# Kernel tuning notes

Hardware: AMD Instinct MI355X
Metric: run time of the kernel (lower is better)

## Reference

```python
import jax, jax.numpy as jnp
import numpy as np

NUM_HEADS = 16
NUM_KV_HEADS = 4
ROPE_THETA = 10000.0


def apply_rope(x, position_ids, theta):
    # x: [B, S, h, d]; position_ids: [B, S]
    d = x.shape[-1]
    freqs = 1.0 / theta ** (jnp.arange(0, d, 2, dtype=jnp.float32) / d)  # [d/2]
    angles = position_ids.astype(jnp.float32)[..., None] * freqs          # [B, S, d/2]
    cos = jnp.cos(angles)[:, :, None, :]                                  # [B, S, 1, d/2]
    sin = jnp.sin(angles)[:, :, None, :]
    xr = x.astype(jnp.float32).reshape(*x.shape[:-1], d // 2, 2)
    x0, x1 = xr[..., 0], xr[..., 1]
    o0 = x0 * cos - x1 * sin
    o1 = x0 * sin + x1 * cos
    out = jnp.stack((o0, o1), axis=-1).reshape(*x.shape)
    return out.astype(x.dtype)


def setup_inputs() -> dict:
    key = jax.random.key(0)
    k0, k1, k2, k3, k4 = jax.random.split(key, 5)
    B, S, H = 1, 2048, 2048
    Hkv = H // (NUM_HEADS // NUM_KV_HEADS)  # 512
    init_scale = 0.02 / np.sqrt(H)
    return {
        "hidden_states": jax.random.normal(k0, (B, S, H), jnp.float32),
        "attention_mask": jnp.ones((B, S), jnp.int32),
        "segment_ids": jnp.zeros((B, S), jnp.int32),
        "position_ids": jnp.broadcast_to(jnp.arange(S, dtype=jnp.int32)[None], (B, S)),
        "Wq": jax.random.normal(k1, (H, H), jnp.float32) * init_scale,
        "Wk": jax.random.normal(k2, (H, Hkv), jnp.float32) * init_scale,
        "Wv": jax.random.normal(k3, (H, Hkv), jnp.float32) * init_scale,
        "Wo": jax.random.normal(k4, (H, H), jnp.float32) * init_scale,
    }


def reference(hidden_states, attention_mask, segment_ids, position_ids, Wq, Wk, Wv, Wo):
    B, S, H = hidden_states.shape
    nh, nkv = NUM_HEADS, NUM_KV_HEADS
    g = nh // nkv
    hd = H // nh

    xq = (hidden_states @ Wq).reshape(B, S, nh, hd)
    xk = (hidden_states @ Wk).reshape(B, S, nkv, hd)
    xv = (hidden_states @ Wv).reshape(B, S, nkv, hd)
    # GQA repeat: 'b s (h d) -> b s (h g) d' == repeat each kv head g times contiguously
    xk = jnp.repeat(xk, g, axis=2)  # [B, S, nh, hd]
    xv = jnp.repeat(xv, g, axis=2)

    xq = apply_rope(xq, position_ids, ROPE_THETA)
    xk = apply_rope(xk, position_ids, ROPE_THETA)

    # masks: causal AND padding AND segment
    causal = jnp.tril(jnp.ones((S, S), dtype=bool))[None, None]            # [1,1,S,S]
    pad = (attention_mask > 0)[:, None, None, :]                            # [B,1,1,S]
    seg = (segment_ids[:, :, None] == segment_ids[:, None, :])[:, None]     # [B,1,S,S]
    mask = causal & pad & seg                                               # [B,1,S,S]

    scale = 1.0 / np.sqrt(hd)
    logits = jnp.einsum("bqhd,bkhd->bhqk", xq.astype(jnp.float32), xk.astype(jnp.float32)) * scale
    logits = jnp.where(mask, logits, jnp.finfo(jnp.float32).min)
    probs = jax.nn.softmax(logits, axis=-1).astype(xv.dtype)
    attn = jnp.einsum("bhqk,bkhd->bqhd", probs, xv)                         # [B,S,nh,hd]

    out = attn.reshape(B, S, H) @ Wo
    return out
```

## Files before the change

### kernel.cpp

```cpp
#include <hip/hip_runtime.h>
#include <hip/hip_bf16.h>
#include <stdint.h>
#include <math.h>

#define SS 2048
#define HH 2048
#define NH 16
#define NKV 4
#define HD 128
#define HKV 512
#define NQKV 3072

typedef __bf16 bf16x8 __attribute__((ext_vector_type(8)));
typedef float f32x4 __attribute__((ext_vector_type(4)));

static_assert(sizeof(bf16x8) == 16, "bf16x8 must be 16B");

__device__ __forceinline__ void async_ld16(const void* gp, void* lp) {
  __builtin_amdgcn_global_load_lds(
      (const __attribute__((address_space(1))) unsigned int*)(uintptr_t)gp,
      (__attribute__((address_space(3))) unsigned int*)(uintptr_t)lp,
      16, 0, 0);
}

__device__ __forceinline__ unsigned short f2bu(float f) {
  __hip_bfloat16 b = __float2bfloat16(f);
  return *reinterpret_cast<unsigned short*>(&b);
}

__global__ __launch_bounds__(256) void k_prep1(
    const float* __restrict__ X, const float* __restrict__ Wq, const float* __restrict__ Wk,
    const float* __restrict__ Wv, const float* __restrict__ Wo,
    const int* __restrict__ amv, const int* __restrict__ seg, int* __restrict__ kseg,
    float2* __restrict__ rtab,
    __hip_bfloat16* __restrict__ Xb, __hip_bfloat16* __restrict__ WqT,
    __hip_bfloat16* __restrict__ WkT, __hip_bfloat16* __restrict__ WvT,
    __hip_bfloat16* __restrict__ WoT) {
  __shared__ float tile[32][33];
  int b = blockIdx.x;
  if (b < 4096) {
    int i = b * 256 + threadIdx.y * 32 + threadIdx.x;
    float4 v = ((const float4*)X)[i];
    ushort4 o;
    o.x = f2bu(v.x); o.y = f2bu(v.y); o.z = f2bu(v.z); o.w = f2bu(v.w);
    ((ushort4*)Xb)[i] = o;
    return;
  }
  b -= 4096;
  if (b >= 10248) {
    int i = (b - 10248) * 256 + threadIdx.y * 32 + threadIdx.x;
    int p = i >> 6, f = i & 63;
    const float L2T_D64 = 0.20762050593046837f;
    float freq = exp2f(-L2T_D64 * (float)f);
    float sn, cs;
    sincosf((float)p * freq, &sn, &cs);
    rtab[i] = make_float2(sn, cs);
    return;
  }
  if (b >= 10240) {
    int i = (b - 10240) * 256 + threadIdx.y * 32 + threadIdx.x;
    kseg[i] = (amv[i] > 0) ? seg[i] : 0x7fffffff;
    return;
  }
  const float* src; __hip_bfloat16* dst; int xtiles;
  if (b < 4096)      { src = Wq; dst = WqT; xtiles = 64; }
  else if (b < 8192) { src = Wo; dst = WoT; xtiles = 64; b -= 4096; }
  else if (b < 9216) { src = Wk; dst = WkT; xtiles = 16; b -= 8192; }
  else               { src = Wv; dst = WvT; xtiles = 16; b -= 9216; }
  const int C = xtiles * 32;
  int bx = (b % xtiles) * 32;
  int by = (b / xtiles) * 32;
  int tx = threadIdx.x, ty = threadIdx.y;
#pragma unroll
  for (int i = 0; i < 4; i++)
    tile[ty + i * 8][tx] = src[(size_t)(by + ty + i * 8) * C + bx + tx];
  __syncthreads();
#pragma unroll
  for (int i = 0; i < 4; i++)
    dst[(size_t)(bx + ty + i * 8) * HH + by + tx] = __float2bfloat16(tile[tx][ty + i * 8]);
}

__global__ __launch_bounds__(256, 2) void k_gemm_qkv(
    const __hip_bfloat16* __restrict__ A, const __hip_bfloat16* __restrict__ B,
    __hip_bfloat16* __restrict__ Qb, __hip_bfloat16* __restrict__ Kb,
    __hip_bfloat16* __restrict__ Vt, const int* __restrict__ pos,
    const float2* __restrict__ rtab) {
  __shared__ __align__(16) __hip_bfloat16 sA0[64 * 64];
  __shared__ __align__(16) __hip_bfloat16 sA1[64 * 64];
  __shared__ __align__(16) __hip_bfloat16 sA2[64 * 64];
  __shared__ __align__(16) __hip_bfloat16 sB0[128 * 64];
  __shared__ __align__(16) __hip_bfloat16 sB1[128 * 64];
  __shared__ __align__(16) __hip_bfloat16 sB2[128 * 64];
  const int tid = threadIdx.x;
  const int lane = tid & 63;
  const int wave = tid >> 6;
  const int bm = blockIdx.y * 64;
  const int bn = blockIdx.x * 128;
  const int wm = (wave & 1) * 32;
  const int wn = (wave >> 1) * 64;
  const int am = lane & 15;
  const int ch = lane >> 4;

  f32x4 acc[2][4] = {};

  auto stage = [&](__hip_bfloat16* sA, __hip_bfloat16* sB, int k0) {
#pragma unroll
    for (int q = 0; q < 2; q++) {
      int c = q * 256 + tid;
      int row = c >> 3, kp = c & 7;
      int col = (kp ^ (row & 7)) * 8;
      async_ld16(A + (size_t)(bm + row) * HH + k0 + col, (char*)sA + c * 16);
    }
#pragma unroll
    for (int q = 0; q < 4; q++) {
      int c = q * 256 + tid;
      int row = c >> 3, kp = c & 7;
      int col = (kp ^ (row & 7)) * 8;
      async_ld16(B + (size_t)(bn + row) * HH + k0 + col, (char*)sB + c * 16);
    }
  };
  auto compute = [&](const __hip_bfloat16* sA, const __hip_bfloat16* sB) {
#pragma unroll
    for (int kb = 0; kb < 2; kb++) {
      bf16x8 a[2], b[4];
#pragma unroll
      for (int i = 0; i < 2; i++) {
        int row = wm + i * 16 + am;
        a[i] = *(const bf16x8*)(sA + row * 64 + (((kb * 4 + ch) ^ (row & 7)) * 8));
      }
#pragma unroll
      for (int j = 0; j < 4; j++) {
        int row = wn + j * 16 + am;
        b[j] = *(const bf16x8*)(sB + row * 64 + (((kb * 4 + ch) ^ (row & 7)) * 8));
      }
#pragma unroll
      for (int i = 0; i < 2; i++)
#pragma unroll
        for (int j = 0; j < 4; j++)
          acc[i][j] = __builtin_amdgcn_mfma_f32_16x16x32_bf16(a[i], b[j], acc[i][j], 0, 0, 0);
    }
  };

  __hip_bfloat16 *cA = sA0, *nA = sA1, *fA = sA2;
  __hip_bfloat16 *cB = sB0, *nB = sB1, *fB = sB2;
  stage(cA, cB, 0);
  stage(nA, nB, 64);
  for (int t = 0; t < 32; ++t) {
    if (t + 1 < 32) asm volatile("s_waitcnt vmcnt(6)" ::: "memory");
    else            asm volatile("s_waitcnt vmcnt(0)" ::: "memory");
    asm volatile("s_barrier" ::: "memory");
    if (t + 2 < 32) stage(fA, fB, (t + 2) * 64);
    compute(cA, cB);
    __hip_bfloat16* tp;
    tp = cA; cA = nA; nA = fA; fA = tp;
    tp = cB; cB = nB; nB = fB; fB = tp;
  }

  const bool isV = (bn >= HH + HKV);
  if (isV) {
#pragma unroll
    for (int j = 0; j < 4; j++) {
      int lc = bn + wn + j * 16 + am - (HH + HKV);
#pragma unroll
      for (int i = 0; i < 2; i++) {
        int row = bm + wm + i * 16 + ch * 4;
        ushort4 o;
        o.x = f2bu(acc[i][j][0]); o.y = f2bu(acc[i][j][1]);
        o.z = f2bu(acc[i][j][2]); o.w = f2bu(acc[i][j][3]);
        *(ushort4*)(Vt + (size_t)lc * SS + row) = o;
      }
    }
  } else {
    const float SCLQ = 0.08838834764831845f * 1.4426950408889634f;
    const bool isQ = (bn < HH);
    int pint[2][4];
#pragma unroll
    for (int i = 0; i < 2; i++)
#pragma unroll
      for (int r = 0; r < 4; r++)
        pint[i][r] = pos[bm + wm + i * 16 + ch * 4 + r];
    const float sgn = (am & 1) ? 1.0f : -1.0f;
#pragma unroll
    for (int j = 0; j < 4; j++) {
      int col = bn + wn + j * 16 + am;
      int lc = isQ ? col : (col - HH);
      int fidx = (lc >> 1) & 63;
#pragma unroll
      for (int i = 0; i < 2; i++)
#pragma unroll
        for (int r = 0; r < 4; r++) {
          float v = acc[i][j][r];
          float px = __shfl_xor(v, 1, 64);
          float2 sc = rtab[pint[i][r] * 64 + fidx];
          float o = v * sc.y + sgn * px * sc.x;
          int row = bm + wm + i * 16 + ch * 4 + r;
          if (isQ) Qb[(size_t)row * HH + col] = __float2bfloat16(o * SCLQ);
          else     Kb[(size_t)row * HKV + lc] = __float2bfloat16(o);
        }
    }
  }
}

__global__ __launch_bounds__(256, 3) void k_gemm_out(
    const __hip_bfloat16* __restrict__ A, const __hip_bfloat16* __restrict__ B,
    float* __restrict__ C) {
  __shared__ __align__(16) __hip_bfloat16 sA0[64 * 64];
  __shared__ __align__(16) __hip_bfloat16 sB0[128 * 64];
  __shared__ __align__(16) __hip_bfloat16 sA1[64 * 64];
  __shared__ __align__(16) __hip_bfloat16 sB1[128 * 64];
  const int tid = threadIdx.x;
  const int lane = tid & 63;
  const int wave = tid >> 6;
  const int bm = blockIdx.y * 64;
  const int bn = blockIdx.x * 128;
  const int wm = (wave & 1) * 32;
  const int wn = (wave >> 1) * 64;
  const int am = lane & 15;
  const int ch = lane >> 4;

  f32x4 acc[2][4] = {};

  auto stage = [&](__hip_bfloat16* sA, __hip_bfloat16* sB, int k0) {
#pragma unroll
    for (int q = 0; q < 2; q++) {
      int c = q * 256 + tid;
      int row = c >> 3, kp = c & 7;
      int col = (kp ^ (row & 7)) * 8;
      async_ld16(A + (size_t)(bm + row) * HH + k0 + col, (char*)sA + c * 16);
    }
#pragma unroll
    for (int q = 0; q < 4; q++) {
      int c = q * 256 + tid;
      int row = c >> 3, kp = c & 7;
      int col = (kp ^ (row & 7)) * 8;
      async_ld16(B + (size_t)(bn + row) * HH + k0 + col, (char*)sB + c * 16);
    }
  };
  auto compute = [&](const __hip_bfloat16* sA, const __hip_bfloat16* sB) {
#pragma unroll
    for (int kb = 0; kb < 2; kb++) {
      bf16x8 a[2], b[4];
#pragma unroll
      for (int i = 0; i < 2; i++) {
        int row = wm + i * 16 + am;
        a[i] = *(const bf16x8*)(sA + row * 64 + (((kb * 4 + ch) ^ (row & 7)) * 8));
      }
#pragma unroll
      for (int j = 0; j < 4; j++) {
        int row = wn + j * 16 + am;
        b[j] = *(const bf16x8*)(sB + row * 64 + (((kb * 4 + ch) ^ (row & 7)) * 8));
      }
#pragma unroll
      for (int i = 0; i < 2; i++)
#pragma unroll
        for (int j = 0; j < 4; j++)
          acc[i][j] = __builtin_amdgcn_mfma_f32_16x16x32_bf16(a[i], b[j], acc[i][j], 0, 0, 0);
    }
  };

  stage(sA0, sB0, 0);
  int k0 = 0;
  while (true) {
    __syncthreads();
    if (k0 + 64 < HH) stage(sA1, sB1, k0 + 64);
    compute(sA0, sB0);
    k0 += 64; if (k0 >= HH) break;
    __syncthreads();
    if (k0 + 64 < HH) stage(sA0, sB0, k0 + 64);
    compute(sA1, sB1);
    k0 += 64; if (k0 >= HH) break;
  }

#pragma unroll
  for (int i = 0; i < 2; i++)
#pragma unroll
    for (int j = 0; j < 4; j++)
#pragma unroll
      for (int r = 0; r < 4; r++) {
        int row = bm + wm + i * 16 + ch * 4 + r;
        int col = bn + wn + j * 16 + am;
        C[(size_t)row * HH + col] = acc[i][j][r];
      }
}

__global__ __launch_bounds__(256, 2) void k_attn(
    const __hip_bfloat16* __restrict__ Qb,
    const __hip_bfloat16* __restrict__ Kb,
    const __hip_bfloat16* __restrict__ Vt,
    const int* __restrict__ seg,
    const int* __restrict__ kseg,
    float* __restrict__ Obuf,
    float* __restrict__ Lbuf) {
  __shared__ __align__(16) __hip_bfloat16 sK[2][64 * 128];
  __shared__ __align__(16) __hip_bfloat16 sV[2][128 * 64];
  __shared__ __align__(16) __hip_bfloat16 sPall[4][16 * 64];

  const int bid = blockIdx.x;
  const int qt = 31 - (bid >> 5);
  const int h = (bid >> 1) & 15;
  const int half = bid & 1;
  const int T = qt + 1;
  const int n0 = (T + 1) >> 1;
  const int kt0 = half ? n0 : 0;
  const int kt1 = half ? T : n0;
  if (kt0 >= kt1) return;

  const int kvh = h >> 2;
  const int tid = threadIdx.x, lane = tid & 63, w = tid >> 6;
  const int am = lane & 15, ch = lane >> 4;
  const int qrow0 = qt * 64 + w * 16;
  char* sP = (char*)&sPall[w][0];

  bf16x8 qf[4];
#pragma unroll
  for (int ks = 0; ks < 4; ks++)
    qf[ks] = *(const bf16x8*)(Qb + (size_t)(qrow0 + am) * HH + h * HD + ks * 32 + ch * 8);

  int segq[4];
#pragma unroll
  for (int r = 0; r < 4; r++) segq[r] = seg[qrow0 + ch * 4 + r];
  const int q0 = seg[qrow0];
  const bool quni = __all((segq[0] == q0) && (segq[1] == q0) &&
                          (segq[2] == q0) && (segq[3] == q0));

  f32x4 o_acc[8] = {};
  float l_s[4] = {0.f, 0.f, 0.f, 0.f};

  auto stage = [&](int kt, int p) {
#pragma unroll
    for (int q = 0; q < 4; q++) {
      int c = q * 256 + tid;
      int row = c >> 4, kp = c & 15;
      int col = (kp ^ (row & 15)) * 8;
      async_ld16(Kb + (size_t)(kt * 64 + row) * HKV + kvh * 128 + col, (char*)sK[p] + c * 16);
    }
#pragma unroll
    for (int q = 0; q < 4; q++) {
      int c = q * 256 + tid;
      int row = c >> 3, kp = c & 7;
      int col = (kp ^ (row & 7)) * 8;
      async_ld16(Vt + (size_t)(kvh * 128 + row) * SS + kt * 64 + col, (char*)sV[p] + c * 16);
    }
  };

  stage(kt0, 0);
  for (int kt = kt0; kt < kt1; kt++) {
    const int p = (kt - kt0) & 1;
    const int kbase = kt * 64;
    __syncthreads();

    int kinfo[4];
#pragma unroll
    for (int jt = 0; jt < 4; jt++) kinfo[jt] = kseg[kbase + jt * 16 + am];

    if (kt + 1 < kt1) stage(kt + 1, p ^ 1);

    f32x4 sacc[4] = {};
    __builtin_amdgcn_s_setprio(1);
#pragma unroll
    for (int ks = 0; ks < 4; ks++)
#pragma unroll
      for (int jt = 0; jt < 4; jt++) {
        bf16x8 kf = *(const bf16x8*)(sK[p] + (jt * 16 + am) * 128 + (((ks * 4 + ch) ^ am) * 8));
        sacc[jt] = __builtin_amdgcn_mfma_f32_16x16x32_bf16(qf[ks], kf, sacc[jt], 0, 0, 0);
      }
    __builtin_amdgcn_s_setprio(0);

    const bool needc = (kbase + 63 > qrow0);
    const bool fast = quni && !needc &&
        __all((kinfo[0] == q0) && (kinfo[1] == q0) &&
              (kinfo[2] == q0) && (kinfo[3] == q0));

    if (fast) {
#pragma unroll
      for (int jt = 0; jt < 4; jt++)
#pragma unroll
        for (int r = 0; r < 4; r++) {
          float pv = exp2f(sacc[jt][r] - 8.0f);
          l_s[r] += pv;
          int row = ch * 4 + r;
          int chunk = (jt * 2 + (am >> 3)) ^ (row & 7);
          *(__hip_bfloat16*)(sP + row * 128 + chunk * 16 + (am & 7) * 2) =
              __float2bfloat16(pv);
        }
    } else {
#pragma unroll
      for (int jt = 0; jt < 4; jt++) {
        int kk = kbase + jt * 16 + am;
#pragma unroll
        for (int r = 0; r < 4; r++) {
          int qrow = qrow0 + ch * 4 + r;
          bool ok = (kinfo[jt] == segq[r]) && (kk <= qrow);
          float pv = ok ? exp2f(sacc[jt][r] - 8.0f) : 0.0f;
          l_s[r] += pv;
          int row = ch * 4 + r;
          int chunk = (jt * 2 + (am >> 3)) ^ (row & 7);
          *(__hip_bfloat16*)(sP + row * 128 + chunk * 16 + (am & 7) * 2) =
              __float2bfloat16(pv);
        }
      }
    }

    __builtin_amdgcn_s_setprio(1);
#pragma unroll
    for (int ks = 0; ks < 2; ks++) {
      bf16x8 pf = *(const bf16x8*)(sP + am * 128 + (((ks * 4 + ch) ^ (am & 7)) * 16));
#pragma unroll
      for (int jt = 0; jt < 8; jt++) {
        int vrow = jt * 16 + am;
        bf16x8 vf = *(const bf16x8*)(sV[p] + vrow * 64 + (((ks * 4 + ch) ^ (vrow & 7)) * 8));
        o_acc[jt] = __builtin_amdgcn_mfma_f32_16x16x32_bf16(pf, vf, o_acc[jt], 0, 0, 0);
      }
    }
    __builtin_amdgcn_s_setprio(0);
  }

#pragma unroll
  for (int off = 1; off < 16; off <<= 1)
#pragma unroll
    for (int r = 0; r < 4; r++) l_s[r] += __shfl_xor(l_s[r], off, 64);
  if (am == 0)
#pragma unroll
    for (int r = 0; r < 4; r++)
      unsafeAtomicAdd(Lbuf + (size_t)(qrow0 + ch * 4 + r) * NH + h, l_s[r]);
#pragma unroll
  for (int jt = 0; jt < 8; jt++)
#pragma unroll
    for (int r = 0; r < 4; r++) {
      int row = qrow0 + ch * 4 + r;
      unsafeAtomicAdd(Obuf + (size_t)row * HH + h * HD + jt * 16 + am, o_acc[jt][r]);
    }
}

__global__ __launch_bounds__(256) void k_norm(
    const float* __restrict__ Obuf, const float* __restrict__ Lbuf,
    __hip_bfloat16* __restrict__ Ab) {
  int i = blockIdx.x * 256 + threadIdx.x;
  int s = i >> 9;
  int hIdx = (i & 511) >> 5;
  float inv = 1.0f / Lbuf[(size_t)s * NH + hIdx];
  float4 v = ((const float4*)Obuf)[i];
  ushort4 o;
  o.x = f2bu(v.x * inv); o.y = f2bu(v.y * inv);
  o.z = f2bu(v.z * inv); o.w = f2bu(v.w * inv);
  ((ushort4*)Ab)[i] = o;
}

extern "C" void kernel_launch(void* const* d_in, const int* in_sizes, int n_in,
                              void* d_out, int out_size, void* d_ws, size_t ws_size,
                              hipStream_t stream) {
  const float* X  = (const float*)d_in[0];
  const int* amv  = (const int*)d_in[1];
  const int* seg  = (const int*)d_in[2];
  const int* pos  = (const int*)d_in[3];
  const float* Wq = (const float*)d_in[4];
  const float* Wk = (const float*)d_in[5];
  const float* Wv = (const float*)d_in[6];
  const float* Wo = (const float*)d_in[7];
  float* out = (float*)d_out;

  char* ws = (char*)d_ws;
  size_t off = 0;
  auto alloc = [&](size_t bytes) { void* p = ws + off; off += (bytes + 255) & ~(size_t)255; return p; };
  __hip_bfloat16* Xb   = (__hip_bfloat16*)alloc((size_t)SS * HH * 2);
  __hip_bfloat16* WqT  = (__hip_bfloat16*)alloc((size_t)HH * HH * 2);
  __hip_bfloat16* WkT  = (__hip_bfloat16*)alloc((size_t)HKV * HH * 2);
  __hip_bfloat16* WvT  = (__hip_bfloat16*)alloc((size_t)HKV * HH * 2);
  __hip_bfloat16* WoT  = (__hip_bfloat16*)alloc((size_t)HH * HH * 2);
  __hip_bfloat16* Qb   = (__hip_bfloat16*)alloc((size_t)SS * HH * 2);
  __hip_bfloat16* Kb   = (__hip_bfloat16*)alloc((size_t)SS * HKV * 2);
  __hip_bfloat16* Vt   = (__hip_bfloat16*)alloc((size_t)HKV * SS * 2);
  __hip_bfloat16* Ab   = (__hip_bfloat16*)alloc((size_t)SS * HH * 2);
  float*          Obuf = (float*)alloc((size_t)SS * HH * 4);
  float*          Lbuf = (float*)alloc((size_t)SS * NH * 4);
  int*            kseg = (int*)alloc((size_t)SS * 4);
  float2*         rtab = (float2*)alloc((size_t)SS * 64 * 8);
  (void)WkT; (void)WvT;

  hipMemsetAsync(Obuf, 0, (size_t)SS * HH * 4 + ((size_t)SS * NH * 4 + 255 & ~(size_t)255), stream);
  k_prep1<<<dim3(14856), dim3(32, 8), 0, stream>>>(X, Wq, Wk, Wv, Wo, amv, seg, kseg, rtab,
                                                   Xb, WqT, WkT, WvT, WoT);
  k_gemm_qkv<<<dim3(NQKV / 128, SS / 64), 256, 0, stream>>>(Xb, WqT, Qb, Kb, Vt, pos, rtab);
  k_attn<<<dim3(1024), 256, 0, stream>>>(Qb, Kb, Vt, seg, kseg, Obuf, Lbuf);
  k_norm<<<dim3(SS * HH / 4 / 256), 256, 0, stream>>>(Obuf, Lbuf, Ab);
  k_gemm_out<<<dim3(HH / 128, SS / 64), 256, 0, stream>>>(Ab, WoT, out);
}
```

Before: 236.5 us.

## Shrink attention key tiles to 32, skip masked tiles per wave, widen transpose tiles

The attention kernel now uses 32-key tiles instead of 64, with smaller LDS buffers and new swizzles, and raises the launch bound so four blocks can share a CU. Each wave also skips QK/PV work on tiles that lie entirely above its causal diagonal. The goal is to cut wasted causal work and improve occupancy, at the cost of more loop iterations and barriers. Separately, the weight transpose in the prep kernel moves to 64x64 tiles with float4 loads and 16-byte bf16 stores, which halves its block count.

```diff
diff --git a/kernel.cpp b/kernel.cpp
--- a/kernel.cpp
+++ b/kernel.cpp
@@ -36,10 +36,11 @@
     __hip_bfloat16* __restrict__ Xb, __hip_bfloat16* __restrict__ WqT,
     __hip_bfloat16* __restrict__ WkT, __hip_bfloat16* __restrict__ WvT,
     __hip_bfloat16* __restrict__ WoT) {
-  __shared__ float tile[32][33];
+  __shared__ __align__(16) __hip_bfloat16 t2[64 * 72];
   int b = blockIdx.x;
+  int t = threadIdx.y * 32 + threadIdx.x;
   if (b < 4096) {
-    int i = b * 256 + threadIdx.y * 32 + threadIdx.x;
+    int i = b * 256 + t;
     float4 v = ((const float4*)X)[i];
     ushort4 o;
     o.x = f2bu(v.x); o.y = f2bu(v.y); o.z = f2bu(v.z); o.w = f2bu(v.w);
@@ -47,8 +48,8 @@
     return;
   }
   b -= 4096;
-  if (b >= 10248) {
-    int i = (b - 10248) * 256 + threadIdx.y * 32 + threadIdx.x;
+  if (b >= 2568) {
+    int i = (b - 2568) * 256 + t;
     int p = i >> 6, f = i & 63;
     const float L2T_D64 = 0.20762050593046837f;
     float freq = exp2f(-L2T_D64 * (float)f);
@@ -57,27 +58,37 @@
     rtab[i] = make_float2(sn, cs);
     return;
   }
-  if (b >= 10240) {
-    int i = (b - 10240) * 256 + threadIdx.y * 32 + threadIdx.x;
+  if (b >= 2560) {
+    int i = (b - 2560) * 256 + t;
     kseg[i] = (amv[i] > 0) ? seg[i] : 0x7fffffff;
     return;
   }
   const float* src; __hip_bfloat16* dst; int xtiles;
-  if (b < 4096)      { src = Wq; dst = WqT; xtiles = 64; }
-  else if (b < 8192) { src = Wo; dst = WoT; xtiles = 64; b -= 4096; }
-  else if (b < 9216) { src = Wk; dst = WkT; xtiles = 16; b -= 8192; }
-  else               { src = Wv; dst = WvT; xtiles = 16; b -= 9216; }
-  const int C = xtiles * 32;
-  int bx = (b % xtiles) * 32;
-  int by = (b / xtiles) * 32;
-  int tx = threadIdx.x, ty = threadIdx.y;
-#pragma unroll
-  for (int i = 0; i < 4; i++)
-    tile[ty + i * 8][tx] = src[(size_t)(by + ty + i * 8) * C + bx + tx];
+  if (b < 1024)      { src = Wq; dst = WqT; xtiles = 32; }
+  else if (b < 2048) { src = Wo; dst = WoT; xtiles = 32; b -= 1024; }
+  else if (b < 2304) { src = Wk; dst = WkT; xtiles = 8;  b -= 2048; }
+  else               { src = Wv; dst = WvT; xtiles = 8;  b -= 2304; }
+  const int C = xtiles * 64;
+  int bx = (b % xtiles) * 64;
+  int by = (b / xtiles) * 64;
+#pragma unroll
+  for (int i = 0; i < 4; i++) {
+    int idx = i * 256 + t;
+    int r = idx >> 4, c4 = (idx & 15) * 4;
+    float4 v = *(const float4*)(src + (size_t)(by + r) * C + bx + c4);
+    t2[(c4 + 0) * 72 + r] = __float2bfloat16(v.x);
+    t2[(c4 + 1) * 72 + r] = __float2bfloat16(v.y);
+    t2[(c4 + 2) * 72 + r] = __float2bfloat16(v.z);
+    t2[(c4 + 3) * 72 + r] = __float2bfloat16(v.w);
+  }
   __syncthreads();
 #pragma unroll
-  for (int i = 0; i < 4; i++)
-    dst[(size_t)(bx + ty + i * 8) * HH + by + tx] = __float2bfloat16(tile[tx][ty + i * 8]);
+  for (int i = 0; i < 2; i++) {
+    int idx = i * 256 + t;
+    int rr = idx >> 3, cc = (idx & 7) * 8;
+    *(bf16x8*)(dst + (size_t)(bx + rr) * HH + by + cc) =
+        *(const bf16x8*)(&t2[rr * 72 + cc]);
+  }
 }
 
 __global__ __launch_bounds__(256, 2) void k_gemm_qkv(
@@ -283,7 +294,7 @@
       }
 }
 
-__global__ __launch_bounds__(256, 2) void k_attn(
+__global__ __launch_bounds__(256, 4) void k_attn(
     const __hip_bfloat16* __restrict__ Qb,
     const __hip_bfloat16* __restrict__ Kb,
     const __hip_bfloat16* __restrict__ Vt,
@@ -291,19 +302,18 @@
     const int* __restrict__ kseg,
     float* __restrict__ Obuf,
     float* __restrict__ Lbuf) {
-  __shared__ __align__(16) __hip_bfloat16 sK[2][64 * 128];
-  __shared__ __align__(16) __hip_bfloat16 sV[2][128 * 64];
-  __shared__ __align__(16) __hip_bfloat16 sPall[4][16 * 64];
+  __shared__ __align__(16) __hip_bfloat16 sK[2][32 * 128];
+  __shared__ __align__(16) __hip_bfloat16 sV[2][128 * 32];
+  __shared__ __align__(16) __hip_bfloat16 sPall[4][16 * 32];
 
   const int bid = blockIdx.x;
   const int qt = 31 - (bid >> 5);
   const int h = (bid >> 1) & 15;
   const int half = bid & 1;
-  const int T = qt + 1;
-  const int n0 = (T + 1) >> 1;
+  const int T = 2 * (qt + 1);
+  const int n0 = qt + 1;
   const int kt0 = half ? n0 : 0;
   const int kt1 = half ? T : n0;
-  if (kt0 >= kt1) return;
 
   const int kvh = h >> 2;
   const int tid = threadIdx.x, lane = tid & 63, w = tid >> 6;
@@ -328,91 +338,92 @@
 
   auto stage = [&](int kt, int p) {
 #pragma unroll
-    for (int q = 0; q < 4; q++) {
+    for (int q = 0; q < 2; q++) {
       int c = q * 256 + tid;
       int row = c >> 4, kp = c & 15;
       int col = (kp ^ (row & 15)) * 8;
-      async_ld16(Kb + (size_t)(kt * 64 + row) * HKV + kvh * 128 + col, (char*)sK[p] + c * 16);
-    }
-#pragma unroll
-    for (int q = 0; q < 4; q++) {
-      int c = q * 256 + tid;
-      int row = c >> 3, kp = c & 7;
-      int col = (kp ^ (row & 7)) * 8;
-      async_ld16(Vt + (size_t)(kvh * 128 + row) * SS + kt * 64 + col, (char*)sV[p] + c * 16);
+      async_ld16(Kb + (size_t)(kt * 32 + row) * HKV + kvh * 128 + col, (char*)sK[p] + c * 16);
+    }
+#pragma unroll
+    for (int q = 0; q < 2; q++) {
+      int c = q * 256 + tid;
+      int row = c >> 2, kp = c & 3;
+      int col = (kp ^ ((row >> 1) & 3)) * 8;
+      async_ld16(Vt + (size_t)(kvh * 128 + row) * SS + kt * 32 + col, (char*)sV[p] + c * 16);
     }
   };
 
   stage(kt0, 0);
   for (int kt = kt0; kt < kt1; kt++) {
     const int p = (kt - kt0) & 1;
-    const int kbase = kt * 64;
+    const int kbase = kt * 32;
+    const bool skip = (kbase > qrow0 + 15);
     __syncthreads();
 
-    int kinfo[4];
-#pragma unroll
-    for (int jt = 0; jt < 4; jt++) kinfo[jt] = kseg[kbase + jt * 16 + am];
-
+    int kinfo[2];
+    if (!skip) {
+#pragma unroll
+      for (int jt = 0; jt < 2; jt++) kinfo[jt] = kseg[kbase + jt * 16 + am];
+    }
     if (kt + 1 < kt1) stage(kt + 1, p ^ 1);
-
-    f32x4 sacc[4] = {};
-    __builtin_amdgcn_s_setprio(1);
-#pragma unroll
-    for (int ks = 0; ks < 4; ks++)
-#pragma unroll
-      for (int jt = 0; jt < 4; jt++) {
-        bf16x8 kf = *(const bf16x8*)(sK[p] + (jt * 16 + am) * 128 + (((ks * 4 + ch) ^ am) * 8));
-        sacc[jt] = __builtin_amdgcn_mfma_f32_16x16x32_bf16(qf[ks], kf, sacc[jt], 0, 0, 0);
-      }
-    __builtin_amdgcn_s_setprio(0);
-
-    const bool needc = (kbase + 63 > qrow0);
-    const bool fast = quni && !needc &&
-        __all((kinfo[0] == q0) && (kinfo[1] == q0) &&
-              (kinfo[2] == q0) && (kinfo[3] == q0));
-
-    if (fast) {
-#pragma unroll
-      for (int jt = 0; jt < 4; jt++)
-#pragma unroll
-        for (int r = 0; r < 4; r++) {
-          float pv = exp2f(sacc[jt][r] - 8.0f);
-          l_s[r] += pv;
-          int row = ch * 4 + r;
-          int chunk = (jt * 2 + (am >> 3)) ^ (row & 7);
-          *(__hip_bfloat16*)(sP + row * 128 + chunk * 16 + (am & 7) * 2) =
-              __float2bfloat16(pv);
+    if (!skip) {
+      f32x4 sacc[2] = {};
+      __builtin_amdgcn_s_setprio(1);
+#pragma unroll
+      for (int ks = 0; ks < 4; ks++)
+#pragma unroll
+        for (int jt = 0; jt < 2; jt++) {
+          bf16x8 kf = *(const bf16x8*)(sK[p] + (jt * 16 + am) * 128 + (((ks * 4 + ch) ^ am) * 8));
+          sacc[jt] = __builtin_amdgcn_mfma_f32_16x16x32_bf16(qf[ks], kf, sacc[jt], 0, 0, 0);
         }
-    } else {
-#pragma unroll
-      for (int jt = 0; jt < 4; jt++) {
-        int kk = kbase + jt * 16 + am;
-#pragma unroll
-        for (int r = 0; r < 4; r++) {
-          int qrow = qrow0 + ch * 4 + r;
-          bool ok = (kinfo[jt] == segq[r]) && (kk <= qrow);
-          float pv = ok ? exp2f(sacc[jt][r] - 8.0f) : 0.0f;
-          l_s[r] += pv;
-          int row = ch * 4 + r;
-          int chunk = (jt * 2 + (am >> 3)) ^ (row & 7);
-          *(__hip_bfloat16*)(sP + row * 128 + chunk * 16 + (am & 7) * 2) =
-              __float2bfloat16(pv);
+      __builtin_amdgcn_s_setprio(0);
+
+      const bool needc = (kbase + 31 > qrow0);
+      const bool fast = quni && !needc &&
+          __all((kinfo[0] == q0) && (kinfo[1] == q0));
+
+      if (fast) {
+#pragma unroll
+        for (int jt = 0; jt < 2; jt++)
+#pragma unroll
+          for (int r = 0; r < 4; r++) {
+            float pv = exp2f(sacc[jt][r] - 8.0f);
+            l_s[r] += pv;
+            int row = ch * 4 + r;
+            int chunk = (jt * 2 + (am >> 3)) ^ (row & 3);
+            *(__hip_bfloat16*)(sP + row * 64 + chunk * 16 + (am & 7) * 2) =
+                __float2bfloat16(pv);
+          }
+      } else {
+#pragma unroll
+        for (int jt = 0; jt < 2; jt++) {
+          int kk = kbase + jt * 16 + am;
+#pragma unroll
+          for (int r = 0; r < 4; r++) {
+            int qrow = qrow0 + ch * 4 + r;
+            bool ok = (kinfo[jt] == segq[r]) && (kk <= qrow);
+            float pv = ok ? exp2f(sacc[jt][r] - 8.0f) : 0.0f;
+            l_s[r] += pv;
+            int row = ch * 4 + r;
+            int chunk = (jt * 2 + (am >> 3)) ^ (row & 3);
+            *(__hip_bfloat16*)(sP + row * 64 + chunk * 16 + (am & 7) * 2) =
+                __float2bfloat16(pv);
+          }
         }
       }
-    }
-
-    __builtin_amdgcn_s_setprio(1);
-#pragma unroll
-    for (int ks = 0; ks < 2; ks++) {
-      bf16x8 pf = *(const bf16x8*)(sP + am * 128 + (((ks * 4 + ch) ^ (am & 7)) * 16));
-#pragma unroll
-      for (int jt = 0; jt < 8; jt++) {
-        int vrow = jt * 16 + am;
-        bf16x8 vf = *(const bf16x8*)(sV[p] + vrow * 64 + (((ks * 4 + ch) ^ (vrow & 7)) * 8));
-        o_acc[jt] = __builtin_amdgcn_mfma_f32_16x16x32_bf16(pf, vf, o_acc[jt], 0, 0, 0);
-      }
-    }
-    __builtin_amdgcn_s_setprio(0);
+
+      __builtin_amdgcn_s_setprio(1);
+      {
+        bf16x8 pf = *(const bf16x8*)(sP + am * 64 + ((ch ^ (am & 3)) * 16));
+#pragma unroll
+        for (int jt = 0; jt < 8; jt++) {
+          int vrow = jt * 16 + am;
+          bf16x8 vf = *(const bf16x8*)(sV[p] + vrow * 32 + ((ch ^ ((vrow >> 1) & 3)) * 8));
+          o_acc[jt] = __builtin_amdgcn_mfma_f32_16x16x32_bf16(pf, vf, o_acc[jt], 0, 0, 0);
+        }
+      }
+      __builtin_amdgcn_s_setprio(0);
+    }
   }
 
 #pragma unroll
@@ -478,8 +489,8 @@
   (void)WkT; (void)WvT;
 
   hipMemsetAsync(Obuf, 0, (size_t)SS * HH * 4 + ((size_t)SS * NH * 4 + 255 & ~(size_t)255), stream);
-  k_prep1<<<dim3(14856), dim3(32, 8), 0, stream>>>(X, Wq, Wk, Wv, Wo, amv, seg, kseg, rtab,
-                                                   Xb, WqT, WkT, WvT, WoT);
+  k_prep1<<<dim3(7176), dim3(32, 8), 0, stream>>>(X, Wq, Wk, Wv, Wo, amv, seg, kseg, rtab,
+                                                  Xb, WqT, WkT, WvT, WoT);
   k_gemm_qkv<<<dim3(NQKV / 128, SS / 64), 256, 0, stream>>>(Xb, WqT, Qb, Kb, Vt, pos, rtab);
   k_attn<<<dim3(1024), 256, 0, stream>>>(Qb, Kb, Vt, seg, kseg, Obuf, Lbuf);
   k_norm<<<dim3(SS * HH / 4 / 256), 256, 0, stream>>>(Obuf, Lbuf, Ab);
```

Result: no change. 234.0 us (-1.0%).
